# Kernel optimization log

Hardware: AMD Instinct MI355X
Metric: run time of the kernel (lower is better)

## Reference

```python
import jax, jax.numpy as jnp
import numpy as np
import math

NQ, NK, QDIM, MDIM, VDIM = 8192, 8192, 512, 512, 512
NEG = -float(1 << 32)


def setup_inputs() -> dict:
    key = jax.random.key(0)
    ks = jax.random.split(key, 8)
    Q = jax.random.normal(ks[0], (NQ, QDIM), dtype=jnp.float32)
    K = jax.random.normal(ks[1], (NK, QDIM), dtype=jnp.float32)
    V = jax.random.normal(ks[2], (NK, VDIM), dtype=jnp.float32)
    mask = jax.random.randint(ks[3], (NQ, NK), 0, 2) == 1
    s = 1.0 / math.sqrt(QDIM)
    WQ_w = jax.random.uniform(ks[4], (MDIM, QDIM), minval=-s, maxval=s, dtype=jnp.float32)
    WQ_b = jax.random.uniform(ks[5], (MDIM,), minval=-s, maxval=s, dtype=jnp.float32)
    WK_w = jax.random.uniform(ks[6], (MDIM, QDIM), minval=-s, maxval=s, dtype=jnp.float32)
    WK_b = jax.random.uniform(ks[7], (MDIM,), minval=-s, maxval=s, dtype=jnp.float32)
    return {"Q": Q, "K": K, "V": V, "WQ_w": WQ_w, "WQ_b": WQ_b,
            "WK_w": WK_w, "WK_b": WK_b, "mask": mask}


def reference(Q, K, V, WQ_w, WQ_b, WK_w, WK_b, mask):
    # Linear projections: y = x @ W^T + b
    Qp = Q @ WQ_w.T + WQ_b          # [NQ, MDIM]
    Kp = K @ WK_w.T + WK_b          # [NK, MDIM]
    scale = 1.0 / math.sqrt(MDIM)
    attn = (Qp @ Kp.T) * scale      # [NQ, NK]
    attn = jnp.where(mask, NEG, attn)
    attn = jax.nn.softmax(attn, axis=-1)
    return attn @ V                 # [NQ, VDIM]
```

## Files before the change

### kernel.cpp

```cpp
#include <hip/hip_runtime.h>

typedef __attribute__((ext_vector_type(8))) short short8;
typedef __attribute__((ext_vector_type(4))) float f32x4;

#define DEVFN __device__ __forceinline__

constexpr float SCALE_ATTN = 0.04419417382415922f;
constexpr float NEGF = -4294967296.0f;

DEVFN unsigned short f2bf(float f) {
  unsigned int u = __float_as_uint(f);
  u += 0x7FFFu + ((u >> 16) & 1u);
  return (unsigned short)(u >> 16);
}
DEVFN float bf2f(unsigned short h) { return __uint_as_float((unsigned)h << 16); }

DEVFN void gl_lds16(const void* g, void* l) {
  __builtin_amdgcn_global_load_lds(
      (const __attribute__((address_space(1))) unsigned int*)g,
      (__attribute__((address_space(3))) unsigned int*)l, 16, 0, 0);
}

DEVFN float dpp_fmax16(float x) {
  int v;
  v = __builtin_amdgcn_update_dpp(0, __float_as_int(x), 0xB1, 0xF, 0xF, true);
  x = fmaxf(x, __int_as_float(v));
  v = __builtin_amdgcn_update_dpp(0, __float_as_int(x), 0x4E, 0xF, 0xF, true);
  x = fmaxf(x, __int_as_float(v));
  v = __builtin_amdgcn_update_dpp(0, __float_as_int(x), 0x141, 0xF, 0xF, true);
  x = fmaxf(x, __int_as_float(v));
  v = __builtin_amdgcn_update_dpp(0, __float_as_int(x), 0x140, 0xF, 0xF, true);
  x = fmaxf(x, __int_as_float(v));
  return x;
}
DEVFN float dpp_fadd16(float x) {
  int v;
  v = __builtin_amdgcn_update_dpp(0, __float_as_int(x), 0xB1, 0xF, 0xF, true);
  x += __int_as_float(v);
  v = __builtin_amdgcn_update_dpp(0, __float_as_int(x), 0x4E, 0xF, 0xF, true);
  x += __int_as_float(v);
  v = __builtin_amdgcn_update_dpp(0, __float_as_int(x), 0x141, 0xF, 0xF, true);
  x += __int_as_float(v);
  v = __builtin_amdgcn_update_dpp(0, __float_as_int(x), 0x140, 0xF, 0xF, true);
  x += __int_as_float(v);
  return x;
}

__global__ void k_detect(const unsigned int* __restrict__ q, const unsigned int* __restrict__ m,
                         int* __restrict__ fflag, int* __restrict__ esize) {
  int lane = threadIdx.x;
  if (blockIdx.x == 0) {
    unsigned bad = 0;
    for (int i = 0; i < 64; i++) {
      unsigned v = q[i * 64 + lane];
      unsigned h = v & 0xFFFFu;
      unsigned e = (h >> 7) & 0xFFu;
      if (h != 0u && (e < 96u || e > 150u)) bad = 1;
    }
    unsigned long long anyb = __ballot(bad != 0);
    if (lane == 0) *fflag = (anyb == 0ULL) ? 1 : 0;
  } else {
    unsigned okd = 1, okh = 1, okb = 1;
    for (int i = 0; i < 64; i++) {
      unsigned v = m[i * 64 + lane];
      if (v > 1u && v != 0x3F800000u) okd = 0;
      unsigned h0 = v & 0xFFFFu, h1 = v >> 16;
      if ((h0 && h0 != 0x3F80u && h0 != 1u) || (h1 && h1 != 0x3F80u && h1 != 1u)) okh = 0;
      if (v & 0xFEFEFEFEu) okb = 0;
    }
    okd = (__ballot(okd == 0) == 0ULL);
    okh = (__ballot(okh == 0) == 0ULL);
    okb = (__ballot(okb == 0) == 0ULL);
    if (lane == 0) *esize = okd ? 4 : (okh ? 2 : 1);
  }
}

__global__ void k_prep(const void* __restrict__ Q, unsigned short* __restrict__ Qb,
                       const void* __restrict__ K, unsigned short* __restrict__ Kb,
                       const void* __restrict__ Wq, unsigned short* __restrict__ Wqb,
                       const void* __restrict__ Wk, unsigned short* __restrict__ Wkb,
                       const void* __restrict__ bq, unsigned short* __restrict__ bqb,
                       const void* __restrict__ bk, unsigned short* __restrict__ bkb,
                       const int* __restrict__ bf16flag) {
  int blk = blockIdx.x;
  const void* src; unsigned short* dst; int base, n;
  if (blk < 2048)      { src = Q;  dst = Qb;  base = blk;        n = 8192 * 512; }
  else if (blk < 4096) { src = K;  dst = Kb;  base = blk - 2048; n = 8192 * 512; }
  else if (blk < 4224) { src = Wq; dst = Wqb; base = blk - 4096; n = 512 * 512; }
  else if (blk < 4352) { src = Wk; dst = Wkb; base = blk - 4224; n = 512 * 512; }
  else if (blk == 4352){ src = bq; dst = bqb; base = 0;          n = 512; }
  else                 { src = bk; dst = bkb; base = 0;          n = 512; }
  int i = (base * 256 + threadIdx.x) * 8;
  if (i >= n) return;
  if (*bf16flag) {
    *(uint4*)(dst + i) = *(const uint4*)((const unsigned short*)src + i);
  } else {
    const float* f = (const float*)src + i;
    float4 a = *(const float4*)f, b = *(const float4*)(f + 4);
    uint4 o;
    o.x = (unsigned)f2bf(a.x) | ((unsigned)f2bf(a.y) << 16);
    o.y = (unsigned)f2bf(a.z) | ((unsigned)f2bf(a.w) << 16);
    o.z = (unsigned)f2bf(b.x) | ((unsigned)f2bf(b.y) << 16);
    o.w = (unsigned)f2bf(b.z) | ((unsigned)f2bf(b.w) << 16);
    *(uint4*)(dst + i) = o;
  }
}

__global__ void k_transpose_v(const void* __restrict__ Vsrc, const int* __restrict__ bf16flag,
                              unsigned short* __restrict__ Vt) {
  __shared__ unsigned short T[64][72];
  int t = threadIdx.x;
  int rb = blockIdx.x, cb = blockIdx.y;
  int r = t >> 3, c8 = (t & 7) * 8;
  int isbf = *bf16flag;
#pragma unroll
  for (int j = 0; j < 2; j++) {
    int row = rb * 64 + j * 32 + r;
    unsigned short e[8];
    if (isbf) {
      alignas(16) unsigned short tmp[8];
      *(uint4*)tmp = *(const uint4*)((const unsigned short*)Vsrc + (size_t)row * 512 + cb * 64 + c8);
#pragma unroll
      for (int i = 0; i < 8; i++) e[i] = tmp[i];
    } else {
      const float* f = (const float*)Vsrc + (size_t)row * 512 + cb * 64 + c8;
      float4 a = *(const float4*)f, b = *(const float4*)(f + 4);
      e[0] = f2bf(a.x); e[1] = f2bf(a.y); e[2] = f2bf(a.z); e[3] = f2bf(a.w);
      e[4] = f2bf(b.x); e[5] = f2bf(b.y); e[6] = f2bf(b.z); e[7] = f2bf(b.w);
    }
#pragma unroll
    for (int i = 0; i < 8; i++) T[c8 + i][j * 32 + r] = e[i];
  }
  __syncthreads();
#pragma unroll
  for (int j = 0; j < 2; j++) {
    int d = cb * 64 + j * 32 + r;
    alignas(16) unsigned short o[8];
#pragma unroll
    for (int i = 0; i < 8; i++) o[i] = T[j * 32 + r][c8 + i];
    int tt = rb * 2 + (c8 >> 5);
    *(uint4*)(Vt + ((size_t)tt * 512 + d) * 32 + (c8 & 31)) = *(const uint4*)o;
  }
}

DEVFN unsigned nib4(unsigned v) {
  unsigned t = v; t |= t >> 1; t |= t >> 2; t |= t >> 4; t &= 0x01010101u;
  return (t * 0x10204080u) >> 28;
}
DEVFN unsigned pair2(unsigned v) {
  unsigned t = v; t |= t >> 8; t |= t >> 4; t |= t >> 2; t |= t >> 1;
  return (t & 1u) | (((t >> 16) & 1u) << 1);
}
__global__ void k_pack(const void* __restrict__ mask, const int* __restrict__ esize,
                       unsigned long long* __restrict__ bits) {
  int wv = (blockIdx.x * blockDim.x + threadIdx.x) >> 6;
  int lane = threadIdx.x & 63;
  int sz = *esize;
  if (sz == 4) {
    const unsigned int* m = (const unsigned int*)mask;
    for (int g = wv; g < 262144; g += 4096) {
      size_t base = (size_t)g * 256 + lane;
      unsigned v0 = m[base], v1 = m[base + 64], v2 = m[base + 128], v3 = m[base + 192];
      unsigned long long b0 = __ballot(v0 != 0u);
      unsigned long long b1 = __ballot(v1 != 0u);
      unsigned long long b2 = __ballot(v2 != 0u);
      unsigned long long b3 = __ballot(v3 != 0u);
      if (lane == 0) {
        bits[g * 4 + 0] = b0; bits[g * 4 + 1] = b1;
        bits[g * 4 + 2] = b2; bits[g * 4 + 3] = b3;
      }
    }
  } else if (sz == 2) {
    const uint4* m = (const uint4*)mask;
    for (int g = wv; g < 131072; g += 4096) {
      uint4 v = m[(size_t)g * 64 + lane];
      unsigned c8 = pair2(v.x) | (pair2(v.y) << 2) | (pair2(v.z) << 4) | (pair2(v.w) << 6);
      unsigned long long x = (unsigned long long)c8 << ((lane & 7) * 8);
      x |= __shfl_xor(x, 1); x |= __shfl_xor(x, 2); x |= __shfl_xor(x, 4);
      if ((lane & 7) == 0) bits[g * 8 + (lane >> 3)] = x;
    }
  } else {
    const uint4* m = (const uint4*)mask;
    for (int g = wv; g < 65536; g += 4096) {
      uint4 v = m[(size_t)g * 64 + lane];
      unsigned c16 = nib4(v.x) | (nib4(v.y) << 4) | (nib4(v.z) << 8) | (nib4(v.w) << 12);
      unsigned long long x = (unsigned long long)c16 << ((lane & 3) * 16);
      x |= __shfl_xor(x, 1); x |= __shfl_xor(x, 2);
      if ((lane & 3) == 0) bits[g * 16 + (lane >> 2)] = x;
    }
  }
}

__global__ __launch_bounds__(256, 2) void k_proj(
    const unsigned short* __restrict__ Aq, const unsigned short* __restrict__ Wq,
    const unsigned short* __restrict__ bq, unsigned short* __restrict__ outq,
    const unsigned short* __restrict__ Ak, const unsigned short* __restrict__ Wk,
    const unsigned short* __restrict__ bk, unsigned short* __restrict__ outk) {
  const unsigned short* A = blockIdx.z ? Ak : Aq;
  const unsigned short* W = blockIdx.z ? Wk : Wq;
  const unsigned short* bias = blockIdx.z ? bk : bq;
  unsigned short* out = blockIdx.z ? outk : outq;

  __shared__ alignas(16) unsigned short As[128 * 64];
  __shared__ alignas(16) unsigned short Bs[128 * 64];
  int tid = threadIdx.x, lane = tid & 63, wave = tid >> 6;
  int wi = wave >> 1, wj = wave & 1;
  int l15 = lane & 15, l4 = lane >> 4;
  int rowbase = blockIdx.x * 128, colbase = blockIdx.y * 128;
  f32x4 acc[4][4];
#pragma unroll
  for (int i = 0; i < 4; i++)
#pragma unroll
    for (int j = 0; j < 4; j++) acc[i][j] = f32x4{0.f, 0.f, 0.f, 0.f};

  int swr = l15 & 7;
  for (int kb = 0; kb < 512; kb += 64) {
    __syncthreads();
#pragma unroll
    for (int t = 0; t < 4; t++) {
      int inst = wave * 4 + t;
      int r = inst * 8 + (lane >> 3);
      int c = ((lane & 7) ^ (r & 7)) * 8;
      gl_lds16(A + (size_t)(rowbase + r) * 512 + kb + c, &As[inst * 512]);
      gl_lds16(W + (size_t)(colbase + r) * 512 + kb + c, &Bs[inst * 512]);
    }
    __syncthreads();
#pragma unroll
    for (int t2 = 0; t2 < 2; t2++) {
      short8 a[4], b[4];
#pragma unroll
      for (int i = 0; i < 4; i++) {
        int row = wi * 64 + i * 16 + l15;
        a[i] = *(const short8*)&As[row * 64 + (((t2 * 4 + l4) ^ swr) * 8)];
      }
#pragma unroll
      for (int j = 0; j < 4; j++) {
        int row = wj * 64 + j * 16 + l15;
        b[j] = *(const short8*)&Bs[row * 64 + (((t2 * 4 + l4) ^ swr) * 8)];
      }
#pragma unroll
      for (int i = 0; i < 4; i++)
#pragma unroll
        for (int j = 0; j < 4; j++)
          acc[i][j] = __builtin_amdgcn_mfma_f32_16x16x32_bf16(a[i], b[j], acc[i][j], 0, 0, 0);
    }
  }
#pragma unroll
  for (int j = 0; j < 4; j++) {
    int col = colbase + wj * 64 + j * 16 + l15;
    float bj = bf2f(bias[col]);
#pragma unroll
    for (int i = 0; i < 4; i++) {
      int row0 = rowbase + wi * 64 + i * 16 + l4 * 4;
#pragma unroll
      for (int r = 0; r < 4; r++)
        out[(size_t)(row0 + r) * 512 + col] = f2bf(acc[i][j][r] + bj);
    }
  }
}

__global__ __launch_bounds__(512, 2) void k_attn(
    const unsigned short* __restrict__ Qp, const unsigned short* __restrict__ Kp,
    const unsigned short* __restrict__ Vt, const unsigned long long* __restrict__ mbits,
    unsigned short* __restrict__ Opart, float* __restrict__ mpart, float* __restrict__ lpart) {
  __shared__ alignas(16) unsigned short KB[2][16384];
  __shared__ alignas(16) unsigned short VB[16384];
  __shared__ alignas(16) unsigned short P2[2][4][128][8];
  __shared__ alignas(16) float alds[2][128];
  __shared__ alignas(16) int nfl[2][8];
  int tid = threadIdx.x, lane = tid & 63, wave = tid >> 6;
  int l15 = lane & 15, l4 = lane >> 4;
  int b = blockIdx.x;
  int split = b & 7;
  int qb = (b >> 3) * 128;

  short8 qf[16];
  {
    int row = qb + wave * 16 + l15;
#pragma unroll
    for (int t = 0; t < 16; t++)
      qf[t] = *(const short8*)(Qp + (size_t)row * 512 + t * 32 + l4 * 8);
  }
  f32x4 o[8][4];
#pragma unroll
  for (int i = 0; i < 8; i++)
#pragma unroll
    for (int j = 0; j < 4; j++) o[i][j] = f32x4{0.f, 0.f, 0.f, 0.f};
  float mi[4] = {NEGF, NEGF, NEGF, NEGF};
  float li[4] = {0.f, 0.f, 0.f, 0.f};

  int swK = l15 | ((l15 & 3) << 4);
  const unsigned int* mb32 = (const unsigned int*)mbits;

  {
    int tv = split * 32;
#pragma unroll
    for (int t = 0; t < 4; t++) {
      int r = wave * 4 + t;
      int swz = (r & 15) | ((r & 3) << 4);
      gl_lds16(Kp + (size_t)(tv * 32 + r) * 512 + ((lane ^ swz) * 8), &KB[0][r * 512]);
    }
  }
  __builtin_amdgcn_s_waitcnt(0x0F70);
  __builtin_amdgcn_s_barrier();

  for (int it = 0; it < 32; it++) {
    int cur = it & 1, prv = cur ^ 1;
    int tv = split * 32 + it;

    unsigned mw[4];
#pragma unroll
    for (int r = 0; r < 4; r++)
      mw[r] = mb32[((size_t)(qb + wave * 16 + l4 * 4 + r) * 128 + split * 16 + (it >> 1)) * 2 + (it & 1)];
    asm volatile("" ::: "memory");

    {
      int tv1 = (it < 31) ? tv + 1 : tv;
#pragma unroll
      for (int t = 0; t < 4; t++) {
        int r = wave * 4 + t;
        int swz = (r & 15) | ((r & 3) << 4);
        gl_lds16(Kp + (size_t)(tv1 * 32 + r) * 512 + ((lane ^ swz) * 8), &KB[prv][r * 512]);
      }
    }

    if (it) {
      __builtin_amdgcn_s_waitcnt(0x0F78);
      __builtin_amdgcn_sched_barrier(0);
      {
        const int4* n4 = (const int4*)&nfl[prv][0];
        int4 na = n4[0], nb4 = n4[1];
        if (na.x | na.y | na.z | na.w | nb4.x | nb4.y | nb4.z | nb4.w) {
#pragma unroll
          for (int rf = 0; rf < 8; rf++) {
            f32x4 av = *(const f32x4*)&alds[prv][rf * 16 + l4 * 4];
#pragma unroll
            for (int df = 0; df < 4; df++)
#pragma unroll
              for (int j = 0; j < 4; j++) o[rf][df][j] *= av[j];
          }
        }
      }
      short8 vf[4];
#pragma unroll
      for (int df = 0; df < 4; df++) {
        int d = wave * 64 + df * 16 + l15;
        vf[df] = *(const short8*)&VB[d * 32 + ((l4 ^ ((l15 >> 2) & 3)) * 8)];
      }
      __builtin_amdgcn_s_setprio(1);
#pragma unroll
      for (int rf = 0; rf < 8; rf++) {
        short8 pa = *(const short8*)&P2[prv][l4][rf * 16 + l15][0];
#pragma unroll
        for (int df = 0; df < 4; df++)
          o[rf][df] = __builtin_amdgcn_mfma_f32_16x16x32_bf16(pa, vf[df], o[rf][df], 0, 0, 0);
      }
      __builtin_amdgcn_s_setprio(0);
    }

#pragma unroll
    for (int t = 0; t < 4; t++) {
      int inst = wave * 4 + t;
      int d = inst * 16 + (lane >> 2);
      int cg = (lane & 3) ^ ((d >> 2) & 3);
      gl_lds16(Vt + (size_t)tv * 16384 + d * 32 + cg * 8, &VB[inst * 512]);
    }

    f32x4 sacc[2];
#pragma unroll
    for (int c = 0; c < 2; c++) sacc[c] = f32x4{0.f, 0.f, 0.f, 0.f};
    __builtin_amdgcn_s_setprio(1);
#pragma unroll
    for (int t2 = 0; t2 < 16; t2++) {
      short8 a = qf[t2];
#pragma unroll
      for (int c = 0; c < 2; c++) {
        int row = c * 16 + l15;
        short8 bb = *(const short8*)&KB[cur][row * 512 + (((t2 * 4 + l4) ^ swK) * 8)];
        sacc[c] = __builtin_amdgcn_mfma_f32_16x16x32_bf16(a, bb, sacc[c], 0, 0, 0);
      }
    }
    __builtin_amdgcn_s_setprio(0);

#pragma unroll
    for (int c = 0; c < 2; c++)
#pragma unroll
      for (int r = 0; r < 4; r++) {
        float s = sacc[c][r] * SCALE_ATTN;
        bool msk = (mw[r] >> (c * 16 + l15)) & 1u;
        sacc[c][r] = msk ? NEGF : s;
      }

    float al4[4];
    bool need = false;
#pragma unroll
    for (int r = 0; r < 4; r++) {
      float t = dpp_fmax16(fmaxf(sacc[0][r], sacc[1][r]));
      al4[r] = t;
      need |= (t > mi[r] + 8.0f);
    }
    unsigned long long blt = __ballot(need);
    if (lane == 0) nfl[cur][wave] = (blt != 0ULL) ? 1 : 0;
    if (blt) {
#pragma unroll
      for (int r = 0; r < 4; r++) {
        float mn = fmaxf(mi[r], al4[r]);
        float a = __expf(mi[r] - mn);
        li[r] *= a;
        mi[r] = mn;
        al4[r] = a;
      }
    } else {
#pragma unroll
      for (int r = 0; r < 4; r++) al4[r] = 1.0f;
    }
    if (l15 == 0) *(f32x4*)&alds[cur][wave * 16 + l4 * 4] = f32x4{al4[0], al4[1], al4[2], al4[3]};

#pragma unroll
    for (int c = 0; c < 2; c++)
#pragma unroll
      for (int r = 0; r < 4; r++) sacc[c][r] = __expf(sacc[c][r] - mi[r]);
#pragma unroll
    for (int r = 0; r < 4; r++)
      li[r] += dpp_fadd16(sacc[0][r] + sacc[1][r]);

#pragma unroll
    for (int r = 0; r < 4; r++) {
      int prow = wave * 16 + l4 * 4 + r;
#pragma unroll
      for (int c = 0; c < 2; c++)
        P2[cur][c * 2 + (l15 >> 3)][prow][l15 & 7] = f2bf(sacc[c][r]);
    }

    __builtin_amdgcn_s_waitcnt(0x0074);
    __builtin_amdgcn_s_barrier();
  }

  __builtin_amdgcn_s_waitcnt(0x0F70);
  __builtin_amdgcn_sched_barrier(0);
  {
    const int4* n4 = (const int4*)&nfl[1][0];
    int4 na = n4[0], nb4 = n4[1];
    if (na.x | na.y | na.z | na.w | nb4.x | nb4.y | nb4.z | nb4.w) {
#pragma unroll
      for (int rf = 0; rf < 8; rf++) {
        f32x4 av = *(const f32x4*)&alds[1][rf * 16 + l4 * 4];
#pragma unroll
        for (int df = 0; df < 4; df++)
#pragma unroll
          for (int j = 0; j < 4; j++) o[rf][df][j] *= av[j];
      }
    }
    short8 vf[4];
#pragma unroll
    for (int df = 0; df < 4; df++) {
      int d = wave * 64 + df * 16 + l15;
      vf[df] = *(const short8*)&VB[d * 32 + ((l4 ^ ((l15 >> 2) & 3)) * 8)];
    }
#pragma unroll
    for (int rf = 0; rf < 8; rf++) {
      short8 pa = *(const short8*)&P2[1][l4][rf * 16 + l15][0];
#pragma unroll
      for (int df = 0; df < 4; df++)
        o[rf][df] = __builtin_amdgcn_mfma_f32_16x16x32_bf16(pa, vf[df], o[rf][df], 0, 0, 0);
    }
  }

#pragma unroll
  for (int r = 0; r < 4; r++) {
    int row = qb + wave * 16 + l4 * 4 + r;
    if (l15 == 0) {
      mpart[(size_t)split * 8192 + row] = mi[r];
      lpart[(size_t)split * 8192 + row] = li[r];
    }
  }
  uint2* op2 = (uint2*)Opart;
#pragma unroll
  for (int rf = 0; rf < 8; rf++)
#pragma unroll
    for (int df = 0; df < 4; df++) {
      int f = wave * 4 + df;
      uint2 v;
      v.x = (unsigned)f2bf(o[rf][df][0]) | ((unsigned)f2bf(o[rf][df][1]) << 16);
      v.y = (unsigned)f2bf(o[rf][df][2]) | ((unsigned)f2bf(o[rf][df][3]) << 16);
      op2[(((size_t)b * 32 + f) * 8 + rf) * 64 + l4 * 16 + l15] = v;
    }
}

__global__ void k_combine(const unsigned short* __restrict__ Opart,
                          const float* __restrict__ mpart, const float* __restrict__ lpart,
                          float* __restrict__ out) {
  int q = blockIdx.x;
  int half = blockIdx.y;
  int tid = threadIdx.x;
  int wave = tid >> 6, lane = tid & 63, l4 = (lane >> 4) & 3, l15 = lane & 15;
  int row0 = q * 128 + wave * 16 + l4 * 4;

  float w[8][4], inv[4];
#pragma unroll
  for (int r = 0; r < 4; r++) {
    float M = NEGF;
    float mv[8];
#pragma unroll
    for (int s = 0; s < 8; s++) { mv[s] = mpart[s * 8192 + row0 + r]; M = fmaxf(M, mv[s]); }
    float L = 0.f;
#pragma unroll
    for (int s = 0; s < 8; s++) {
      float ws = __expf(mv[s] - M);
      w[s][r] = ws;
      L += ws * lpart[s * 8192 + row0 + r];
    }
    inv[r] = 1.0f / L;
  }
  const uint2* op2 = (const uint2*)Opart;
#pragma unroll
  for (int fo = 0; fo < 16; fo++) {
    int f = half * 16 + fo;
    float acc[4] = {0.f, 0.f, 0.f, 0.f};
#pragma unroll
    for (int s = 0; s < 8; s++) {
      uint2 v = op2[(((size_t)(q * 8 + s) * 32 + f) * 8 + wave) * 64 + l4 * 16 + l15];
      acc[0] += w[s][0] * bf2f((unsigned short)(v.x & 0xFFFFu));
      acc[1] += w[s][1] * bf2f((unsigned short)(v.x >> 16));
      acc[2] += w[s][2] * bf2f((unsigned short)(v.y & 0xFFFFu));
      acc[3] += w[s][3] * bf2f((unsigned short)(v.y >> 16));
    }
    int col = f * 16 + l15;
#pragma unroll
    for (int r = 0; r < 4; r++)
      out[(size_t)(row0 + r) * 512 + col] = acc[r] * inv[r];
  }
}

extern "C" void kernel_launch(void* const* d_in, const int* in_sizes, int n_in,
                              void* d_out, int out_size, void* d_ws, size_t ws_size,
                              hipStream_t stream) {
  const void* Q   = d_in[0];
  const void* K   = d_in[1];
  const void* V   = d_in[2];
  const void* WQw = d_in[3];
  const void* WQb = d_in[4];
  const void* WKw = d_in[5];
  const void* WKb = d_in[6];
  const void* mask = d_in[7];
  float* out = (float*)d_out;
  char* ws = (char*)d_ws;
  (void)in_sizes; (void)n_in; (void)out_size; (void)ws_size;

  constexpr size_t SZ_MAT = (size_t)8192 * 512 * 2;
  size_t off = 4096;
  unsigned short* Qb  = (unsigned short*)(ws + off); off += SZ_MAT;
  unsigned short* Kb  = (unsigned short*)(ws + off); off += SZ_MAT;
  unsigned short* Wqb = (unsigned short*)(ws + off); off += (size_t)512 * 512 * 2;
  unsigned short* Wkb = (unsigned short*)(ws + off); off += (size_t)512 * 512 * 2;
  unsigned short* bqb = (unsigned short*)(ws + off); off += 1024;
  unsigned short* bkb = (unsigned short*)(ws + off); off += 1024;
  unsigned short* Vt  = (unsigned short*)(ws + off); off += SZ_MAT;
  unsigned short* Qp  = (unsigned short*)(ws + off); off += SZ_MAT;
  unsigned short* Kp  = (unsigned short*)(ws + off); off += SZ_MAT;
  unsigned long long* mbits = (unsigned long long*)(ws + off); off += (size_t)8192 * 128 * 8;
  unsigned short* Opart = (unsigned short*)(ws + off); off += (size_t)512 * 512 * 32 * 8;
  float* mpart = (float*)(ws + off); off += (size_t)8 * 8192 * 4;
  float* lpart = (float*)(ws + off); off += (size_t)8 * 8192 * 4;
  int* fflag = (int*)ws;
  int* esize = (int*)(ws + 64);

  k_detect<<<2, 64, 0, stream>>>((const unsigned int*)Q, (const unsigned int*)mask, fflag, esize);
  k_prep<<<4354, 256, 0, stream>>>(Q, Qb, K, Kb, WQw, Wqb, WKw, Wkb, WQb, bqb, WKb, bkb, fflag);
  k_transpose_v<<<dim3(128, 8), 256, 0, stream>>>(V, fflag, Vt);
  k_pack<<<1024, 256, 0, stream>>>(mask, esize, mbits);
  k_proj<<<dim3(64, 4, 2), 256, 0, stream>>>(Qb, Wqb, bqb, Qp, Kb, Wkb, bkb, Kp);
  k_attn<<<512, 512, 0, stream>>>(Qp, Kp, Vt, mbits, Opart, mpart, lpart);
  k_combine<<<dim3(64, 2), 512, 0, stream>>>(Opart, mpart, lpart, out);
}
```

Baseline: 791.7 us.

## Interleave softmax with PV MFMAs and fold scale·log2e into Q projection

Restructures the attention loop so the QK^T tile for the current step is computed before the deferred P·V MFMAs. The row-max, rescale and exp work is then interleaved between the PV MFMA groups so VALU and matrix work overlap. The softmax scale times log2(e) is folded into the Q projection epilogue, and __expf is replaced by raw v_exp_f32 (exp2). The per-lane row-sum reduction is deferred to the end of the loop. The lazy-rescale threshold is raised from 8 to 11.5 in log2 units, and the first iteration is peeled out of the loop. The risks are bf16 rounding of the scaled Q and higher register pressure from interleaving.

```diff
diff --git a/kernel.cpp b/kernel.cpp
--- a/kernel.cpp
+++ b/kernel.cpp
@@ -5,8 +5,8 @@
 
 #define DEVFN __device__ __forceinline__
 
-constexpr float SCALE_ATTN = 0.04419417382415922f;
 constexpr float NEGF = -4294967296.0f;
+constexpr float SCALE_LOG2E = 0.06375872f;
 
 DEVFN unsigned short f2bf(float f) {
   unsigned int u = __float_as_uint(f);
@@ -14,6 +14,12 @@
   return (unsigned short)(u >> 16);
 }
 DEVFN float bf2f(unsigned short h) { return __uint_as_float((unsigned)h << 16); }
+
+DEVFN float exp2v(float x) {
+  float r;
+  asm("v_exp_f32 %0, %1" : "=v"(r) : "v"(x));
+  return r;
+}
 
 DEVFN void gl_lds16(const void* g, void* l) {
   __builtin_amdgcn_global_load_lds(
@@ -200,6 +206,7 @@
   const unsigned short* W = blockIdx.z ? Wk : Wq;
   const unsigned short* bias = blockIdx.z ? bk : bq;
   unsigned short* out = blockIdx.z ? outk : outq;
+  float sc = blockIdx.z ? 1.0f : SCALE_LOG2E;
 
   __shared__ alignas(16) unsigned short As[128 * 64];
   __shared__ alignas(16) unsigned short Bs[128 * 64];
@@ -254,7 +261,7 @@
       int row0 = rowbase + wi * 64 + i * 16 + l4 * 4;
 #pragma unroll
       for (int r = 0; r < 4; r++)
-        out[(size_t)(row0 + r) * 512 + col] = f2bf(acc[i][j][r] + bj);
+        out[(size_t)(row0 + r) * 512 + col] = f2bf((acc[i][j][r] + bj) * sc);
     }
   }
 }
@@ -287,126 +294,82 @@
 #pragma unroll
     for (int j = 0; j < 4; j++) o[i][j] = f32x4{0.f, 0.f, 0.f, 0.f};
   float mi[4] = {NEGF, NEGF, NEGF, NEGF};
-  float li[4] = {0.f, 0.f, 0.f, 0.f};
+  float li_l[4] = {0.f, 0.f, 0.f, 0.f};
 
   int swK = l15 | ((l15 & 3) << 4);
   const unsigned int* mb32 = (const unsigned int*)mbits;
 
-  {
-    int tv = split * 32;
-#pragma unroll
-    for (int t = 0; t < 4; t++) {
-      int r = wave * 4 + t;
-      int swz = (r & 15) | ((r & 3) << 4);
-      gl_lds16(Kp + (size_t)(tv * 32 + r) * 512 + ((lane ^ swz) * 8), &KB[0][r * 512]);
-    }
-  }
+#define STAGE_K(TV, BUF)                                                         \
+  {                                                                              \
+    _Pragma("unroll") for (int t = 0; t < 4; t++) {                              \
+      int r = wave * 4 + t;                                                      \
+      int swz = (r & 15) | ((r & 3) << 4);                                       \
+      gl_lds16(Kp + (size_t)((TV) * 32 + r) * 512 + ((lane ^ swz) * 8),          \
+               &KB[BUF][r * 512]);                                               \
+    }                                                                            \
+  }
+#define STAGE_V(TV)                                                              \
+  {                                                                              \
+    _Pragma("unroll") for (int t = 0; t < 4; t++) {                              \
+      int inst = wave * 4 + t;                                                   \
+      int d = inst * 16 + (lane >> 2);                                           \
+      int cg = (lane & 3) ^ ((d >> 2) & 3);                                      \
+      gl_lds16(Vt + (size_t)(TV) * 16384 + d * 32 + cg * 8, &VB[inst * 512]);    \
+    }                                                                            \
+  }
+#define LOAD_MASKS(IT)                                                           \
+  _Pragma("unroll") for (int r = 0; r < 4; r++)                                  \
+    mw[r] = mb32[((size_t)(qb + wave * 16 + l4 * 4 + r) * 128 + split * 16 +     \
+                  ((IT) >> 1)) * 2 + ((IT) & 1)];
+#define QKT(BUF)                                                                 \
+  {                                                                              \
+    _Pragma("unroll") for (int c = 0; c < 2; c++) sacc[c] = f32x4{0.f,0.f,0.f,0.f}; \
+    __builtin_amdgcn_s_setprio(1);                                               \
+    _Pragma("unroll") for (int t2 = 0; t2 < 16; t2++) {                          \
+      short8 a = qf[t2];                                                         \
+      _Pragma("unroll") for (int c = 0; c < 2; c++) {                            \
+        int row = c * 16 + l15;                                                  \
+        short8 bb = *(const short8*)&KB[BUF][row * 512 + (((t2 * 4 + l4) ^ swK) * 8)]; \
+        sacc[c] = __builtin_amdgcn_mfma_f32_16x16x32_bf16(a, bb, sacc[c], 0, 0, 0); \
+      }                                                                          \
+    }                                                                            \
+    __builtin_amdgcn_s_setprio(0);                                               \
+  }
+#define MASK_APPLY()                                                             \
+  _Pragma("unroll") for (int c = 0; c < 2; c++)                                  \
+    _Pragma("unroll") for (int r = 0; r < 4; r++) {                              \
+      bool msk = (mw[r] >> (c * 16 + l15)) & 1u;                                 \
+      sacc[c][r] = msk ? NEGF : sacc[c][r];                                      \
+    }
+
+  STAGE_K(split * 32, 0);
   __builtin_amdgcn_s_waitcnt(0x0F70);
   __builtin_amdgcn_s_barrier();
 
-  for (int it = 0; it < 32; it++) {
-    int cur = it & 1, prv = cur ^ 1;
-    int tv = split * 32 + it;
-
+  {
+    const int tv = split * 32;
     unsigned mw[4];
-#pragma unroll
-    for (int r = 0; r < 4; r++)
-      mw[r] = mb32[((size_t)(qb + wave * 16 + l4 * 4 + r) * 128 + split * 16 + (it >> 1)) * 2 + (it & 1)];
-    asm volatile("" ::: "memory");
-
-    {
-      int tv1 = (it < 31) ? tv + 1 : tv;
-#pragma unroll
-      for (int t = 0; t < 4; t++) {
-        int r = wave * 4 + t;
-        int swz = (r & 15) | ((r & 3) << 4);
-        gl_lds16(Kp + (size_t)(tv1 * 32 + r) * 512 + ((lane ^ swz) * 8), &KB[prv][r * 512]);
-      }
-    }
-
-    if (it) {
-      __builtin_amdgcn_s_waitcnt(0x0F78);
-      __builtin_amdgcn_sched_barrier(0);
-      {
-        const int4* n4 = (const int4*)&nfl[prv][0];
-        int4 na = n4[0], nb4 = n4[1];
-        if (na.x | na.y | na.z | na.w | nb4.x | nb4.y | nb4.z | nb4.w) {
-#pragma unroll
-          for (int rf = 0; rf < 8; rf++) {
-            f32x4 av = *(const f32x4*)&alds[prv][rf * 16 + l4 * 4];
-#pragma unroll
-            for (int df = 0; df < 4; df++)
-#pragma unroll
-              for (int j = 0; j < 4; j++) o[rf][df][j] *= av[j];
-          }
-        }
-      }
-      short8 vf[4];
-#pragma unroll
-      for (int df = 0; df < 4; df++) {
-        int d = wave * 64 + df * 16 + l15;
-        vf[df] = *(const short8*)&VB[d * 32 + ((l4 ^ ((l15 >> 2) & 3)) * 8)];
-      }
-      __builtin_amdgcn_s_setprio(1);
-#pragma unroll
-      for (int rf = 0; rf < 8; rf++) {
-        short8 pa = *(const short8*)&P2[prv][l4][rf * 16 + l15][0];
-#pragma unroll
-        for (int df = 0; df < 4; df++)
-          o[rf][df] = __builtin_amdgcn_mfma_f32_16x16x32_bf16(pa, vf[df], o[rf][df], 0, 0, 0);
-      }
-      __builtin_amdgcn_s_setprio(0);
-    }
-
-#pragma unroll
-    for (int t = 0; t < 4; t++) {
-      int inst = wave * 4 + t;
-      int d = inst * 16 + (lane >> 2);
-      int cg = (lane & 3) ^ ((d >> 2) & 3);
-      gl_lds16(Vt + (size_t)tv * 16384 + d * 32 + cg * 8, &VB[inst * 512]);
-    }
-
+    LOAD_MASKS(0);
+    STAGE_K(tv + 1, 1);
     f32x4 sacc[2];
-#pragma unroll
-    for (int c = 0; c < 2; c++) sacc[c] = f32x4{0.f, 0.f, 0.f, 0.f};
-    __builtin_amdgcn_s_setprio(1);
-#pragma unroll
-    for (int t2 = 0; t2 < 16; t2++) {
-      short8 a = qf[t2];
-#pragma unroll
-      for (int c = 0; c < 2; c++) {
-        int row = c * 16 + l15;
-        short8 bb = *(const short8*)&KB[cur][row * 512 + (((t2 * 4 + l4) ^ swK) * 8)];
-        sacc[c] = __builtin_amdgcn_mfma_f32_16x16x32_bf16(a, bb, sacc[c], 0, 0, 0);
-      }
-    }
-    __builtin_amdgcn_s_setprio(0);
-
-#pragma unroll
-    for (int c = 0; c < 2; c++)
-#pragma unroll
-      for (int r = 0; r < 4; r++) {
-        float s = sacc[c][r] * SCALE_ATTN;
-        bool msk = (mw[r] >> (c * 16 + l15)) & 1u;
-        sacc[c][r] = msk ? NEGF : s;
-      }
-
+    QKT(0);
+    MASK_APPLY();
     float al4[4];
     bool need = false;
 #pragma unroll
     for (int r = 0; r < 4; r++) {
       float t = dpp_fmax16(fmaxf(sacc[0][r], sacc[1][r]));
       al4[r] = t;
-      need |= (t > mi[r] + 8.0f);
+      need |= (t > mi[r] + 11.5f);
     }
     unsigned long long blt = __ballot(need);
-    if (lane == 0) nfl[cur][wave] = (blt != 0ULL) ? 1 : 0;
+    if (lane == 0) nfl[0][wave] = (blt != 0ULL) ? 1 : 0;
     if (blt) {
 #pragma unroll
       for (int r = 0; r < 4; r++) {
         float mn = fmaxf(mi[r], al4[r]);
-        float a = __expf(mi[r] - mn);
-        li[r] *= a;
+        float a = exp2v(mi[r] - mn);
+        li_l[r] *= a;
         mi[r] = mn;
         al4[r] = a;
       }
@@ -414,24 +377,120 @@
 #pragma unroll
       for (int r = 0; r < 4; r++) al4[r] = 1.0f;
     }
-    if (l15 == 0) *(f32x4*)&alds[cur][wave * 16 + l4 * 4] = f32x4{al4[0], al4[1], al4[2], al4[3]};
-
-#pragma unroll
-    for (int c = 0; c < 2; c++)
-#pragma unroll
-      for (int r = 0; r < 4; r++) sacc[c][r] = __expf(sacc[c][r] - mi[r]);
-#pragma unroll
-    for (int r = 0; r < 4; r++)
-      li[r] += dpp_fadd16(sacc[0][r] + sacc[1][r]);
-
+    if (l15 == 0) *(f32x4*)&alds[0][wave * 16 + l4 * 4] = f32x4{al4[0], al4[1], al4[2], al4[3]};
+#pragma unroll
+    for (int r = 0; r < 4; r++) {
+      sacc[0][r] = exp2v(sacc[0][r] - mi[r]);
+      sacc[1][r] = exp2v(sacc[1][r] - mi[r]);
+      li_l[r] += sacc[0][r] + sacc[1][r];
+    }
 #pragma unroll
     for (int r = 0; r < 4; r++) {
       int prow = wave * 16 + l4 * 4 + r;
 #pragma unroll
       for (int c = 0; c < 2; c++)
-        P2[cur][c * 2 + (l15 >> 3)][prow][l15 & 7] = f2bf(sacc[c][r]);
-    }
-
+        P2[0][c * 2 + (l15 >> 3)][prow][l15 & 7] = f2bf(sacc[c][r]);
+    }
+    STAGE_V(tv);
+    __builtin_amdgcn_s_waitcnt(0x0074);
+    __builtin_amdgcn_s_barrier();
+  }
+
+  for (int it = 1; it < 32; ++it) {
+    const int cur = it & 1, prv = cur ^ 1;
+    const int tv = split * 32 + it;
+
+    unsigned mw[4];
+    LOAD_MASKS(it);
+    STAGE_K((it < 31) ? tv + 1 : tv, prv);
+
+    f32x4 sacc[2];
+    QKT(cur);
+    MASK_APPLY();
+
+    __builtin_amdgcn_s_waitcnt(0x0F78);
+    __builtin_amdgcn_sched_barrier(0);
+
+    {
+      const int4* n4 = (const int4*)&nfl[prv][0];
+      int4 na = n4[0], nb4 = n4[1];
+      if (na.x | na.y | na.z | na.w | nb4.x | nb4.y | nb4.z | nb4.w) {
+#pragma unroll
+        for (int rf = 0; rf < 8; rf++) {
+          f32x4 av = *(const f32x4*)&alds[prv][rf * 16 + l4 * 4];
+#pragma unroll
+          for (int df = 0; df < 4; df++)
+#pragma unroll
+            for (int j = 0; j < 4; j++) o[rf][df][j] *= av[j];
+        }
+      }
+    }
+    short8 vf[4];
+#pragma unroll
+    for (int df = 0; df < 4; df++) {
+      int d = wave * 64 + df * 16 + l15;
+      vf[df] = *(const short8*)&VB[d * 32 + ((l4 ^ ((l15 >> 2) & 3)) * 8)];
+    }
+
+    float al4[4];
+    bool need = false;
+    unsigned long long blt = 0;
+    __builtin_amdgcn_s_setprio(1);
+#pragma unroll
+    for (int rf = 0; rf < 8; rf++) {
+      short8 pa = *(const short8*)&P2[prv][l4][rf * 16 + l15][0];
+#pragma unroll
+      for (int df = 0; df < 4; df++)
+        o[rf][df] = __builtin_amdgcn_mfma_f32_16x16x32_bf16(pa, vf[df], o[rf][df], 0, 0, 0);
+      if (rf < 4) {
+        const int r = rf;
+        float t = dpp_fmax16(fmaxf(sacc[0][r], sacc[1][r]));
+        al4[r] = t;
+        need |= (t > mi[r] + 11.5f);
+      } else if (rf == 4) {
+        blt = __ballot(need);
+        if (lane == 0) nfl[cur][wave] = (blt != 0ULL) ? 1 : 0;
+        if (blt) {
+#pragma unroll
+          for (int r = 0; r < 4; r++) {
+            float mn = fmaxf(mi[r], al4[r]);
+            float a = exp2v(mi[r] - mn);
+            li_l[r] *= a;
+            mi[r] = mn;
+            al4[r] = a;
+          }
+        } else {
+#pragma unroll
+          for (int r = 0; r < 4; r++) al4[r] = 1.0f;
+        }
+        if (l15 == 0) *(f32x4*)&alds[cur][wave * 16 + l4 * 4] = f32x4{al4[0], al4[1], al4[2], al4[3]};
+      } else if (rf == 5) {
+#pragma unroll
+        for (int r = 0; r < 2; r++) {
+          sacc[0][r] = exp2v(sacc[0][r] - mi[r]);
+          sacc[1][r] = exp2v(sacc[1][r] - mi[r]);
+          li_l[r] += sacc[0][r] + sacc[1][r];
+        }
+      } else if (rf == 6) {
+#pragma unroll
+        for (int r = 2; r < 4; r++) {
+          sacc[0][r] = exp2v(sacc[0][r] - mi[r]);
+          sacc[1][r] = exp2v(sacc[1][r] - mi[r]);
+          li_l[r] += sacc[0][r] + sacc[1][r];
+        }
+      } else {
+#pragma unroll
+        for (int r = 0; r < 4; r++) {
+          int prow = wave * 16 + l4 * 4 + r;
+#pragma unroll
+          for (int c = 0; c < 2; c++)
+            P2[cur][c * 2 + (l15 >> 3)][prow][l15 & 7] = f2bf(sacc[c][r]);
+        }
+      }
+    }
+    __builtin_amdgcn_s_setprio(0);
+
+    STAGE_V(tv);
     __builtin_amdgcn_s_waitcnt(0x0074);
     __builtin_amdgcn_s_barrier();
   }
@@ -466,6 +525,9 @@
     }
   }
 
+  float li[4];
+#pragma unroll
+  for (int r = 0; r < 4; r++) li[r] = dpp_fadd16(li_l[r]);
 #pragma unroll
   for (int r = 0; r < 4; r++) {
     int row = qb + wave * 16 + l4 * 4 + r;
@@ -485,6 +547,11 @@
       v.y = (unsigned)f2bf(o[rf][df][2]) | ((unsigned)f2bf(o[rf][df][3]) << 16);
       op2[(((size_t)b * 32 + f) * 8 + rf) * 64 + l4 * 16 + l15] = v;
     }
+#undef STAGE_K
+#undef STAGE_V
+#undef LOAD_MASKS
+#undef QKT
+#undef MASK_APPLY
 }
 
 __global__ void k_combine(const unsigned short* __restrict__ Opart,
@@ -506,7 +573,7 @@
     float L = 0.f;
 #pragma unroll
     for (int s = 0; s < 8; s++) {
-      float ws = __expf(mv[s] - M);
+      float ws = exp2v(mv[s] - M);
       w[s][r] = ws;
       L += ws * lpart[s * 8192 + row0 + r];
     }
```

Result: slower. 870.0 us (+9.9%).
